# Kernel optimization log

Hardware: AMD Instinct MI355X
Metric: run time of the kernel (lower is better)

Reference implementation:

```python
import jax, jax.numpy as jnp
import numpy as np

B, C, N, V, H = 8, 256, 1024, 12, 4
D = C // H  # 64
BN_EPS = 1e-5
NEG = 1e10


def _vconv(x, W, b, g, bt, m4):
    """VointConv block: 1x1 conv + BN(batch stats) + relu, with reset_voint_mask
    applied after every sublayer (as in the torch loop).
    x: [B, Cin, N, V], W: [Cout, Cin], m4: [B, 1, N, V] float mask."""
    y = (jnp.einsum('oc,bcnv->bonv', W, x) + b[None, :, None, None]) * m4
    mu = jnp.mean(y, axis=(0, 2, 3), keepdims=True)
    var = jnp.var(y, axis=(0, 2, 3), keepdims=True)
    y = ((y - mu) * jax.lax.rsqrt(var + BN_EPS) * g[None, :, None, None]
         + bt[None, :, None, None]) * m4
    return jax.nn.relu(y) * m4


def setup_inputs() -> dict:
    key = jax.random.key(0)
    ks = jax.random.split(key, 20)
    inp = {}
    inp['voints_feats'] = jax.random.normal(ks[0], (B, C, N, V), jnp.float32)
    inp['voints_mask'] = (jax.random.uniform(ks[1], (B, N, V)) > 0.3).astype(jnp.float32)
    w = lambda k, shp: (jax.random.normal(k, shp, jnp.float32) * 0.05)
    # embed_layers[0]: VointConv([C, C/heads])
    inp['We'] = w(ks[2], (D, C)); inp['be'] = w(ks[3], (D,))
    inp['ge'] = 1.0 + 0.1 * jax.random.normal(ks[4], (D,), jnp.float32)
    inp['bne'] = 0.1 * jax.random.normal(ks[5], (D,), jnp.float32)
    # embed_atten_layers[0]: VointConv([C/heads, 3*C])
    inp['Wa'] = w(ks[6], (3 * C, D)); inp['ba'] = w(ks[7], (3 * C,))
    inp['ga'] = 1.0 + 0.1 * jax.random.normal(ks[8], (3 * C,), jnp.float32)
    inp['bna'] = 0.1 * jax.random.normal(ks[9], (3 * C,), jnp.float32)
    # to_out[0]: VointConv([C, C])
    inp['Wo'] = w(ks[10], (C, C)); inp['bo'] = w(ks[11], (C,))
    inp['go'] = 1.0 + 0.1 * jax.random.normal(ks[12], (C,), jnp.float32)
    inp['bno'] = 0.1 * jax.random.normal(ks[13], (C,), jnp.float32)
    # feedforward[0]: VointConv([C, C])
    inp['Wf'] = w(ks[14], (C, C)); inp['bf'] = w(ks[15], (C,))
    inp['gf'] = 1.0 + 0.1 * jax.random.normal(ks[16], (C,), jnp.float32)
    inp['bnf'] = 0.1 * jax.random.normal(ks[17], (C,), jnp.float32)
    return inp


def reference(voints_feats, voints_mask, We, be, ge, bne, Wa, ba, ga, bna,
              Wo, bo, go, bno, Wf, bf, gf, bnf):
    mask = voints_mask                      # [B, N, V] float
    m4 = mask[:, None, :, :]                # [B, 1, N, V]
    # embedding to per-head dim, then joint QKV projection
    emb = _vconv(voints_feats, We, be, ge, bne, m4)      # [B, D, N, V]
    qkv = _vconv(emb, Wa, ba, ga, bna, m4)               # [B, 3C, N, V]
    k, q, v = jnp.split(qkv, 3, axis=1)                  # torch.chunk order: k, q, v
    resh = lambda t: t.reshape(B, H, D, N, V)            # 'b (h d) n v -> b h d n v'
    q, k, v = resh(q), resh(k), resh(v)
    scale = float(C) ** (-0.5)
    dots = jnp.einsum('bhdnv,bhdnj->bhnvj', q, k) * scale  # [B,H,N,V,V]
    empty = jnp.sum(mask, axis=-1) == 0                  # [B, N]
    dots = jnp.where(empty[:, None, :, None, None], 0.0, dots)
    # vointsoftmax: bias broadcasts over query dim v (mask[...,None] -> [B,1,N,V,1])
    qbias = jnp.where(mask[:, None, :, :, None] > 0, 0.0, -NEG)
    attn = jax.nn.softmax(dots + qbias, axis=-1) * mask[:, None, :, :, None]
    # faithful to source: 'b h n v j, b h d n v -> b h n v d' (j summed over attn only)
    out = jnp.einsum('bhnvj,bhdnv->bhnvd', attn, v)      # [B,H,N,V,D]
    out = out.transpose(0, 1, 4, 2, 3).reshape(B, C, N, V)  # 'b h n v d -> b (h d) n v'
    out = jnp.where(empty[:, None, :, None], 0.0, out)
    out = _vconv(out, Wo, bo, go, bno, m4)
    x = voints_feats + out
    x = x + _vconv(x, Wf, bf, gf, bnf, m4)
    return x
```

## Files before the change

kernel.cpp:

```cpp
#include <hip/hip_runtime.h>
#include <hip/hip_bf16.h>

typedef __attribute__((ext_vector_type(8))) __bf16 bf16x8;
typedef __attribute__((ext_vector_type(4))) float floatx4;
typedef __attribute__((ext_vector_type(8))) unsigned short ushort8;

namespace {
constexpr int kC  = 256;
constexpr int kNV = 1024 * 12;
constexpr int kP  = 8 * kNV;
constexpr float kEps = 1e-5f;

constexpr size_t OFF_PARAMS = 0;
constexpr size_t OFF_PART   = 2048;
constexpr size_t OFF_WB     = 2048 + 16384;
constexpr size_t OFF_Y1     = OFF_WB + 81920;
constexpr size_t OFF_Y2     = OFF_Y1 + (size_t)kP * 64 / 2;
constexpr size_t OFF_Y3     = OFF_Y2 + (size_t)kP * 256 / 2;
}

__device__ __forceinline__ unsigned short f2bf(float f) {
    unsigned int u = __builtin_bit_cast(unsigned int, f);
    u += 0x7FFFu + ((u >> 16) & 1u);
    return (unsigned short)(u >> 16);
}
__device__ __forceinline__ float bf2f(unsigned short h) {
    unsigned int u = ((unsigned int)h) << 16;
    return __builtin_bit_cast(float, u);
}

__global__ void convw_kernel(const float* __restrict__ We, const float* __restrict__ Wa,
                             const float* __restrict__ Wo, const float* __restrict__ Wf,
                             unsigned short* __restrict__ dst)
{
    const int f = (blockIdx.x * 256 + threadIdx.x) * 4;
    const float* src; int off;
    if (f < 16384)      { src = We;            off = f; }
    else if (f < 32768) { src = Wa + 512 * 64; off = f - 16384; }
    else if (f < 98304) { src = Wo;            off = f - 32768; }
    else                { src = Wf;            off = f - 98304; }
    const float4 v = *(const float4*)&src[off];
    ushort4 o; o.x = f2bf(v.x); o.y = f2bf(v.y); o.z = f2bf(v.z); o.w = f2bf(v.w);
    *(ushort4*)&dst[f] = o;
}

template<int BM, int MT, int K, int MODE>
__global__ __launch_bounds__(256, 2) void gemm_kernel(
    const unsigned short* __restrict__ Wb, const float* __restrict__ bias,
    const unsigned short* __restrict__ Yprev, const float* __restrict__ X0,
    const float* __restrict__ mask,
    const float* __restrict__ actA, const float* __restrict__ actB,
    unsigned short* __restrict__ Yout, float* __restrict__ partial)
{
    constexpr int LD = 40;
    constexpr int FM = 4;
    constexpr int FP = (BM == 128) ? 4 : 2;
    __shared__ unsigned short As[BM * LD];
    __shared__ unsigned short Bs[128 * LD];
    __shared__ float Ms[128];

    const int tid  = threadIdx.x;
    const int lane = tid & 63, w = tid >> 6, quad = lane >> 4, lt = lane & 15;
    const int mW = (BM == 128) ? (w >> 1) * 64 : 0;
    const int pW = (BM == 128) ? (w & 1) * 64 : w * 32;
    const int pBase = blockIdx.y * 128;
    const int m0g = blockIdx.x * BM;
    const int b  = pBase / kNV;
    const int q0 = pBase - b * kNV;

    if (tid < 128) Ms[tid] = mask[pBase + tid];
    __syncthreads();

    floatx4 acc[FM][FP];
    #pragma unroll
    for (int fm = 0; fm < FM; ++fm)
        #pragma unroll
        for (int fp = 0; fp < FP; ++fp) acc[fm][fp] = (floatx4)0.f;

    constexpr int AI = BM / 64;
    for (int k0 = 0; k0 < K; k0 += 32) {
        ushort8 av[AI];
        #pragma unroll
        for (int i = 0; i < AI; ++i) {
            const int idx = tid + i * 256;
            const int m = idx >> 2, kq = (idx & 3) * 8;
            av[i] = *(const ushort8*)&Wb[(size_t)(m0g + m) * K + k0 + kq];
        }
        float bv[2][8];
        int bp[2], bkq[2];
        #pragma unroll
        for (int i = 0; i < 2; ++i) {
            const int idx = tid + i * 256;
            const int p = idx >> 2, kq = (idx & 3) * 8;
            bp[i] = p; bkq[i] = kq;
            if constexpr (MODE == 0) {
                #pragma unroll
                for (int j = 0; j < 8; ++j)
                    bv[i][j] = X0[(size_t)(b * kC + k0 + kq + j) * kNV + q0 + p];
            } else {
                const ushort8 y8 = *(const ushort8*)&Yprev[(size_t)(pBase + p) * K + k0 + kq];
                const float mp = Ms[p];
                #pragma unroll
                for (int j = 0; j < 8; ++j) {
                    float v = bf2f(y8[j]);
                    v = mp * fmaxf(fmaf(actA[k0 + kq + j], v, actB[k0 + kq + j]), 0.f);
                    if constexpr (MODE == 2)
                        v += X0[(size_t)(b * kC + k0 + kq + j) * kNV + q0 + p];
                    bv[i][j] = v;
                }
            }
        }
        __syncthreads();
        #pragma unroll
        for (int i = 0; i < AI; ++i) {
            const int idx = tid + i * 256;
            *(ushort8*)&As[(idx >> 2) * LD + (idx & 3) * 8] = av[i];
        }
        #pragma unroll
        for (int i = 0; i < 2; ++i) {
            ushort8 o;
            #pragma unroll
            for (int j = 0; j < 8; ++j) o[j] = f2bf(bv[i][j]);
            *(ushort8*)&Bs[bp[i] * LD + bkq[i]] = o;
        }
        __syncthreads();
        bf16x8 aF[FM], bF[FP];
        #pragma unroll
        for (int fm = 0; fm < FM; ++fm)
            aF[fm] = *(const bf16x8*)&As[(mW + fm * 16 + lt) * LD + quad * 8];
        #pragma unroll
        for (int fp = 0; fp < FP; ++fp)
            bF[fp] = *(const bf16x8*)&Bs[(pW + fp * 16 + lt) * LD + quad * 8];
        #pragma unroll
        for (int fm = 0; fm < FM; ++fm)
            #pragma unroll
            for (int fp = 0; fp < FP; ++fp)
                acc[fm][fp] = __builtin_amdgcn_mfma_f32_16x16x32_bf16(aF[fm], bF[fp], acc[fm][fp], 0, 0, 0);
    }

    float mpv[FP];
    #pragma unroll
    for (int fp = 0; fp < FP; ++fp) mpv[fp] = Ms[pW + fp * 16 + lt];
    float sumv[FM][4], sqv[FM][4];
    #pragma unroll
    for (int fm = 0; fm < FM; ++fm)
        #pragma unroll
        for (int i = 0; i < 4; ++i) { sumv[fm][i] = 0.f; sqv[fm][i] = 0.f; }

    #pragma unroll
    for (int fm = 0; fm < FM; ++fm) {
        float bia[4];
        #pragma unroll
        for (int i = 0; i < 4; ++i) bia[i] = bias[m0g + mW + fm * 16 + quad * 4 + i];
        #pragma unroll
        for (int fp = 0; fp < FP; ++fp) {
            const int pG = pBase + pW + fp * 16 + lt;
            float vv[4];
            #pragma unroll
            for (int i = 0; i < 4; ++i) {
                const float v = (acc[fm][fp][i] + bia[i]) * mpv[fp];
                vv[i] = v; sumv[fm][i] += v; sqv[fm][i] += v * v;
            }
            ushort4 o; o.x = f2bf(vv[0]); o.y = f2bf(vv[1]); o.z = f2bf(vv[2]); o.w = f2bf(vv[3]);
            *(ushort4*)&Yout[(size_t)pG * MT + m0g + mW + fm * 16 + quad * 4] = o;
        }
    }
    #pragma unroll
    for (int fm = 0; fm < FM; ++fm)
        #pragma unroll
        for (int i = 0; i < 4; ++i) {
            #pragma unroll
            for (int off = 1; off < 16; off <<= 1) {
                sumv[fm][i] += __shfl_xor(sumv[fm][i], off);
                sqv[fm][i]  += __shfl_xor(sqv[fm][i], off);
            }
        }
    if (lt == 0) {
        float* part = partial + (size_t)(blockIdx.y & 7) * 512;
        #pragma unroll
        for (int fm = 0; fm < FM; ++fm)
            #pragma unroll
            for (int i = 0; i < 4; ++i) {
                const int cG = m0g + mW + fm * 16 + quad * 4 + i;
                atomicAdd(&part[cG], sumv[fm][i]);
                atomicAdd(&part[256 + cG], sqv[fm][i]);
            }
    }
}

__global__ void finalize_kernel(const float* __restrict__ part,
                                const float* __restrict__ g, const float* __restrict__ bt,
                                float* __restrict__ ab, int M)
{
    const int m = blockIdx.x * 64 + threadIdx.x;
    if (m >= M) return;
    float s = 0.f, s2 = 0.f;
    #pragma unroll
    for (int k = 0; k < 8; ++k) { s += part[k * 512 + m]; s2 += part[k * 512 + 256 + m]; }
    const float mu  = s * (1.f / kP);
    const float var = s2 * (1.f / kP) - mu * mu;
    const float A = rsqrtf(var + kEps) * g[m];
    ab[m] = A;
    ab[256 + m] = fmaf(-mu, A, bt[m]);
}

__global__ __launch_bounds__(256) void final_kernel(
    const float* __restrict__ x, const unsigned short* __restrict__ y3,
    const unsigned short* __restrict__ y4,
    const float* __restrict__ p3, const float* __restrict__ p4,
    const float* __restrict__ mask, float* __restrict__ out)
{
    constexpr int TL = 258;
    __shared__ unsigned short T3[32 * TL];
    __shared__ unsigned short T4[32 * TL];
    const int p0 = blockIdx.x * 32;
    const int b  = p0 / kNV;
    const int q0 = p0 - b * kNV;

    #pragma unroll
    for (int i = 0; i < 4; ++i) {
        const int idx = threadIdx.x + i * 256;
        const int p = idx >> 5, c0 = (idx & 31) * 8;
        *(ushort8*)&T3[p * TL + c0] = *(const ushort8*)&y3[(size_t)(p0 + p) * 256 + c0];
        *(ushort8*)&T4[p * TL + c0] = *(const ushort8*)&y4[(size_t)(p0 + p) * 256 + c0];
    }
    __syncthreads();

    const int qv = (threadIdx.x & 15) * 2;
    const int cb = threadIdx.x >> 4;
    const float m0v = mask[p0 + qv], m1v = mask[p0 + qv + 1];
    #pragma unroll
    for (int j = 0; j < 16; ++j) {
        const int c = cb + j * 16;
        const float a3 = p3[c], b3 = p3[256 + c], a4 = p4[c], b4 = p4[256 + c];
        const size_t ro = (size_t)(b * kC + c) * kNV + q0 + qv;
        const float2 xv = *(const float2*)&x[ro];
        const float v30 = bf2f(T3[qv * TL + c]),       v31 = bf2f(T3[(qv + 1) * TL + c]);
        const float v40 = bf2f(T4[qv * TL + c]),       v41 = bf2f(T4[(qv + 1) * TL + c]);
        float2 o;
        o.x = xv.x + m0v * (fmaxf(fmaf(a3, v30, b3), 0.f) + fmaxf(fmaf(a4, v40, b4), 0.f));
        o.y = xv.y + m1v * (fmaxf(fmaf(a3, v31, b3), 0.f) + fmaxf(fmaf(a4, v41, b4), 0.f));
        *(float2*)&out[ro] = o;
    }
}

extern "C" void kernel_launch(void* const* d_in, const int* in_sizes, int n_in,
                              void* d_out, int out_size, void* d_ws, size_t ws_size,
                              hipStream_t stream)
{
    const float* x    = (const float*)d_in[0];
    const float* mask = (const float*)d_in[1];
    const float* We   = (const float*)d_in[2];
    const float* be   = (const float*)d_in[3];
    const float* ge   = (const float*)d_in[4];
    const float* bne  = (const float*)d_in[5];
    const float* Wa   = (const float*)d_in[6];
    const float* ba   = (const float*)d_in[7];
    const float* ga   = (const float*)d_in[8];
    const float* bna  = (const float*)d_in[9];
    const float* Wo   = (const float*)d_in[10];
    const float* bo   = (const float*)d_in[11];
    const float* go   = (const float*)d_in[12];
    const float* bno  = (const float*)d_in[13];
    const float* Wf   = (const float*)d_in[14];
    const float* bf   = (const float*)d_in[15];
    const float* gf   = (const float*)d_in[16];
    const float* bnf  = (const float*)d_in[17];
    float* out = (float*)d_out;
    float* ws  = (float*)d_ws;

    float* params = ws + OFF_PARAMS;
    float* part   = ws + OFF_PART;
    unsigned short* Wb = (unsigned short*)(ws + OFF_WB);
    unsigned short* y1 = (unsigned short*)(ws + OFF_Y1);
    unsigned short* y2 = (unsigned short*)(ws + OFF_Y2);
    unsigned short* y3 = (unsigned short*)(ws + OFF_Y3);

    hipMemsetAsync(part, 0, 16384 * sizeof(float), stream);
    convw_kernel<<<160, 256, 0, stream>>>(We, Wa, Wo, Wf, Wb);

    const dim3 blk(256);
    const int PT = kP / 128;

    gemm_kernel<64, 64, 256, 0><<<dim3(1, PT), blk, 0, stream>>>(
        Wb, be, nullptr, x, mask, nullptr, nullptr, y1, part);
    finalize_kernel<<<1, 64, 0, stream>>>(part, ge, bne, params, 64);

    gemm_kernel<128, 256, 64, 1><<<dim3(2, PT), blk, 0, stream>>>(
        Wb + 16384, ba + 512, y1, nullptr, mask, params, params + 256, y2, part + 4096);
    finalize_kernel<<<4, 64, 0, stream>>>(part + 4096, ga + 512, bna + 512, params + 512, 256);

    gemm_kernel<128, 256, 256, 1><<<dim3(2, PT), blk, 0, stream>>>(
        Wb + 32768, bo, y2, nullptr, mask, params + 512, params + 768, y3, part + 8192);
    finalize_kernel<<<4, 64, 0, stream>>>(part + 8192, go, bno, params + 1024, 256);

    gemm_kernel<128, 256, 256, 2><<<dim3(2, PT), blk, 0, stream>>>(
        Wb + 98304, bf, y3, x, mask, params + 1024, params + 1280, y2, part + 12288);
    finalize_kernel<<<4, 64, 0, stream>>>(part + 12288, gf, bnf, params + 1536, 256);

    final_kernel<<<kP / 32, blk, 0, stream>>>(
        x, y3, y2, params + 1024, params + 1536, mask, out);
}
```

Baseline: 432.1 us.

## Pre-transpose input to point-major bf16 and reuse it across GEMMs and final

A new transpose kernel converts the channel-major fp32 input into a point-major bf16 copy. The first GEMM, the residual-add GEMM and the final epilogue all read this copy with contiguous 16-byte loads. Before, they gathered fp32 values with strided per-element loads. The trade is one extra pass over the input and a larger workspace. The residual added to the output is now the bf16-rounded input rather than the fp32 original, which costs some precision.

```diff
diff --git a/kernel.cpp b/kernel.cpp
--- a/kernel.cpp
+++ b/kernel.cpp
@@ -14,7 +14,8 @@
 constexpr size_t OFF_PARAMS = 0;
 constexpr size_t OFF_PART   = 2048;
 constexpr size_t OFF_WB     = 2048 + 16384;
-constexpr size_t OFF_Y1     = OFF_WB + 81920;
+constexpr size_t OFF_XT     = OFF_WB + 81920;
+constexpr size_t OFF_Y1     = OFF_XT + (size_t)kP * 256 / 2;
 constexpr size_t OFF_Y2     = OFF_Y1 + (size_t)kP * 64 / 2;
 constexpr size_t OFF_Y3     = OFF_Y2 + (size_t)kP * 256 / 2;
 }
@@ -44,10 +45,43 @@
     *(ushort4*)&dst[f] = o;
 }
 
+__global__ __launch_bounds__(256) void transpose_kernel(
+    const float* __restrict__ x, unsigned short* __restrict__ xT)
+{
+    __shared__ float T[64][65];
+    const int p0 = blockIdx.x * 64;
+    const int c0 = blockIdx.y * 64;
+    const int b  = p0 / kNV;
+    const int q0 = p0 - b * kNV;
+    const int t  = threadIdx.x;
+
+    const int cl = t >> 2;
+    const int pq = (t & 3) * 16;
+    const float* src = &x[(size_t)(b * kC + c0 + cl) * kNV + q0 + pq];
+    #pragma unroll
+    for (int i = 0; i < 4; ++i) {
+        const float4 v = *(const float4*)&src[i * 4];
+        T[cl][pq + i * 4 + 0] = v.x;
+        T[cl][pq + i * 4 + 1] = v.y;
+        T[cl][pq + i * 4 + 2] = v.z;
+        T[cl][pq + i * 4 + 3] = v.w;
+    }
+    __syncthreads();
+    const int pr = t >> 2;
+    const int cb = (t & 3) * 16;
+    #pragma unroll
+    for (int i = 0; i < 2; ++i) {
+        ushort8 o;
+        #pragma unroll
+        for (int j = 0; j < 8; ++j) o[j] = f2bf(T[cb + i * 8 + j][pr]);
+        *(ushort8*)&xT[(size_t)(p0 + pr) * 256 + c0 + cb + i * 8] = o;
+    }
+}
+
 template<int BM, int MT, int K, int MODE>
 __global__ __launch_bounds__(256, 2) void gemm_kernel(
     const unsigned short* __restrict__ Wb, const float* __restrict__ bias,
-    const unsigned short* __restrict__ Yprev, const float* __restrict__ X0,
+    const unsigned short* __restrict__ Yprev, const unsigned short* __restrict__ XT,
     const float* __restrict__ mask,
     const float* __restrict__ actA, const float* __restrict__ actB,
     unsigned short* __restrict__ Yout, float* __restrict__ partial)
@@ -65,8 +99,6 @@
     const int pW = (BM == 128) ? (w & 1) * 64 : w * 32;
     const int pBase = blockIdx.y * 128;
     const int m0g = blockIdx.x * BM;
-    const int b  = pBase / kNV;
-    const int q0 = pBase - b * kNV;
 
     if (tid < 128) Ms[tid] = mask[pBase + tid];
     __syncthreads();
@@ -86,7 +118,7 @@
             const int m = idx >> 2, kq = (idx & 3) * 8;
             av[i] = *(const ushort8*)&Wb[(size_t)(m0g + m) * K + k0 + kq];
         }
-        float bv[2][8];
+        ushort8 bsv[2];
         int bp[2], bkq[2];
         #pragma unroll
         for (int i = 0; i < 2; ++i) {
@@ -94,19 +126,19 @@
             const int p = idx >> 2, kq = (idx & 3) * 8;
             bp[i] = p; bkq[i] = kq;
             if constexpr (MODE == 0) {
-                #pragma unroll
-                for (int j = 0; j < 8; ++j)
-                    bv[i][j] = X0[(size_t)(b * kC + k0 + kq + j) * kNV + q0 + p];
+                bsv[i] = *(const ushort8*)&XT[(size_t)(pBase + p) * 256 + k0 + kq];
             } else {
                 const ushort8 y8 = *(const ushort8*)&Yprev[(size_t)(pBase + p) * K + k0 + kq];
+                ushort8 x8;
+                if constexpr (MODE == 2)
+                    x8 = *(const ushort8*)&XT[(size_t)(pBase + p) * 256 + k0 + kq];
                 const float mp = Ms[p];
                 #pragma unroll
                 for (int j = 0; j < 8; ++j) {
                     float v = bf2f(y8[j]);
                     v = mp * fmaxf(fmaf(actA[k0 + kq + j], v, actB[k0 + kq + j]), 0.f);
-                    if constexpr (MODE == 2)
-                        v += X0[(size_t)(b * kC + k0 + kq + j) * kNV + q0 + p];
-                    bv[i][j] = v;
+                    if constexpr (MODE == 2) v += bf2f(x8[j]);
+                    bsv[i][j] = f2bf(v);
                 }
             }
         }
@@ -117,12 +149,8 @@
             *(ushort8*)&As[(idx >> 2) * LD + (idx & 3) * 8] = av[i];
         }
         #pragma unroll
-        for (int i = 0; i < 2; ++i) {
-            ushort8 o;
-            #pragma unroll
-            for (int j = 0; j < 8; ++j) o[j] = f2bf(bv[i][j]);
-            *(ushort8*)&Bs[bp[i] * LD + bkq[i]] = o;
-        }
+        for (int i = 0; i < 2; ++i)
+            *(ushort8*)&Bs[bp[i] * LD + bkq[i]] = bsv[i];
         __syncthreads();
         bf16x8 aF[FM], bF[FP];
         #pragma unroll
@@ -205,12 +233,13 @@
 }
 
 __global__ __launch_bounds__(256) void final_kernel(
-    const float* __restrict__ x, const unsigned short* __restrict__ y3,
+    const unsigned short* __restrict__ xT, const unsigned short* __restrict__ y3,
     const unsigned short* __restrict__ y4,
     const float* __restrict__ p3, const float* __restrict__ p4,
     const float* __restrict__ mask, float* __restrict__ out)
 {
-    constexpr int TL = 258;
+    constexpr int TL = 264;
+    __shared__ unsigned short TX[32 * TL];
     __shared__ unsigned short T3[32 * TL];
     __shared__ unsigned short T4[32 * TL];
     const int p0 = blockIdx.x * 32;
@@ -221,6 +250,7 @@
     for (int i = 0; i < 4; ++i) {
         const int idx = threadIdx.x + i * 256;
         const int p = idx >> 5, c0 = (idx & 31) * 8;
+        *(ushort8*)&TX[p * TL + c0] = *(const ushort8*)&xT[(size_t)(p0 + p) * 256 + c0];
         *(ushort8*)&T3[p * TL + c0] = *(const ushort8*)&y3[(size_t)(p0 + p) * 256 + c0];
         *(ushort8*)&T4[p * TL + c0] = *(const ushort8*)&y4[(size_t)(p0 + p) * 256 + c0];
     }
@@ -234,12 +264,12 @@
         const int c = cb + j * 16;
         const float a3 = p3[c], b3 = p3[256 + c], a4 = p4[c], b4 = p4[256 + c];
         const size_t ro = (size_t)(b * kC + c) * kNV + q0 + qv;
-        const float2 xv = *(const float2*)&x[ro];
+        const float x0v = bf2f(TX[qv * TL + c]),       x1v = bf2f(TX[(qv + 1) * TL + c]);
         const float v30 = bf2f(T3[qv * TL + c]),       v31 = bf2f(T3[(qv + 1) * TL + c]);
         const float v40 = bf2f(T4[qv * TL + c]),       v41 = bf2f(T4[(qv + 1) * TL + c]);
         float2 o;
-        o.x = xv.x + m0v * (fmaxf(fmaf(a3, v30, b3), 0.f) + fmaxf(fmaf(a4, v40, b4), 0.f));
-        o.y = xv.y + m1v * (fmaxf(fmaf(a3, v31, b3), 0.f) + fmaxf(fmaf(a4, v41, b4), 0.f));
+        o.x = x0v + m0v * (fmaxf(fmaf(a3, v30, b3), 0.f) + fmaxf(fmaf(a4, v40, b4), 0.f));
+        o.y = x1v + m1v * (fmaxf(fmaf(a3, v31, b3), 0.f) + fmaxf(fmaf(a4, v41, b4), 0.f));
         *(float2*)&out[ro] = o;
     }
 }
@@ -272,18 +302,20 @@
     float* params = ws + OFF_PARAMS;
     float* part   = ws + OFF_PART;
     unsigned short* Wb = (unsigned short*)(ws + OFF_WB);
+    unsigned short* xT = (unsigned short*)(ws + OFF_XT);
     unsigned short* y1 = (unsigned short*)(ws + OFF_Y1);
     unsigned short* y2 = (unsigned short*)(ws + OFF_Y2);
     unsigned short* y3 = (unsigned short*)(ws + OFF_Y3);
 
     hipMemsetAsync(part, 0, 16384 * sizeof(float), stream);
     convw_kernel<<<160, 256, 0, stream>>>(We, Wa, Wo, Wf, Wb);
+    transpose_kernel<<<dim3(kP / 64, 4), 256, 0, stream>>>(x, xT);
 
     const dim3 blk(256);
     const int PT = kP / 128;
 
     gemm_kernel<64, 64, 256, 0><<<dim3(1, PT), blk, 0, stream>>>(
-        Wb, be, nullptr, x, mask, nullptr, nullptr, y1, part);
+        Wb, be, nullptr, xT, mask, nullptr, nullptr, y1, part);
     finalize_kernel<<<1, 64, 0, stream>>>(part, ge, bne, params, 64);
 
     gemm_kernel<128, 256, 64, 1><<<dim3(2, PT), blk, 0, stream>>>(
@@ -295,9 +327,9 @@
     finalize_kernel<<<4, 64, 0, stream>>>(part + 8192, go, bno, params + 1024, 256);
 
     gemm_kernel<128, 256, 256, 2><<<dim3(2, PT), blk, 0, stream>>>(
-        Wb + 98304, bf, y3, x, mask, params + 1024, params + 1280, y2, part + 12288);
+        Wb + 98304, bf, y3, xT, mask, params + 1024, params + 1280, y2, part + 12288);
     finalize_kernel<<<4, 64, 0, stream>>>(part + 12288, gf, bnf, params + 1536, 256);
 
     final_kernel<<<kP / 32, blk, 0, stream>>>(
-        x, y3, y2, params + 1024, params + 1536, mask, out);
-}
+        xT, y3, y2, params + 1024, params + 1536, mask, out);
+}
```

After: 441.8 us. 1.02x slower.
